# Kernel optimization log

Measured on AMD Instinct MI355X. Metric: run time of the kernel, lower is better.

Reference implementation:

```python
import jax, jax.numpy as jnp
import numpy as np

B, T, DIM, H, BUCKET = 4, 4096, 1024, 16, 64
E = DIM // H          # head dim = 64
U = T // BUCKET       # number of buckets = 64
EPS = 1e-6


def setup_inputs() -> dict:
    key = jax.random.key(0)
    ks = jax.random.split(key, 5)
    scale = 1.0 / np.sqrt(DIM)
    return {
        "x": jax.random.normal(ks[0], (B, T, DIM), dtype=jnp.float32),
        "Wq": jax.random.normal(ks[1], (DIM, DIM), dtype=jnp.float32) * scale,
        "Wk": jax.random.normal(ks[2], (DIM, DIM), dtype=jnp.float32) * scale,
        "Wv": jax.random.normal(ks[3], (DIM, DIM), dtype=jnp.float32) * scale,
        "Wo": jax.random.normal(ks[4], (DIM, DIM), dtype=jnp.float32) * scale,
        "bo": jnp.zeros((DIM,), dtype=jnp.float32),
    }


def _causal_linear_attn(q, k, v):
    # q, k, v: [b, h, t, e]; psi(k) = elu(k) + 1; q softmaxed over feature dim
    q = jax.nn.softmax(q, axis=-1)
    k = jax.nn.elu(k) + 1.0
    bucket = lambda x: x.reshape(*x.shape[:-2], U, BUCKET, E)  # [b,h,u,n,e]
    b_q, b_k, b_v = bucket(q), bucket(k), bucket(v)
    # cumulative key sums per bucket: [b,h,u,d]
    b_k_cumsum = jnp.cumsum(b_k.sum(axis=-2), axis=2)
    # per-bucket context then cumulative over buckets: [b,h,u,d,e]
    context = jnp.einsum("bhund,bhune->bhude", b_k, b_v)
    context = jnp.cumsum(context, axis=2)
    context = context / (b_k_cumsum[..., None] + EPS)
    # shift by one bucket (blindspot): bucket u sees context through bucket u-1
    context = jnp.concatenate(
        [jnp.zeros_like(context[:, :, :1]), context[:, :, :-1]], axis=2
    )
    attn = jnp.einsum("bhund,bhude->bhune", b_q, context)
    return attn.reshape(q.shape)  # [b,h,t,e]


def reference(x, Wq, Wk, Wv, Wo, bo):
    b, t, _ = x.shape
    q = x @ Wq
    k = x @ Wk
    v = x @ Wv
    merge = lambda z: z.reshape(b, t, H, E).transpose(0, 2, 1, 3)  # [b,h,t,e]
    attn = _causal_linear_attn(merge(q), merge(k), merge(v))
    out = attn.transpose(0, 2, 1, 3).reshape(b, t, DIM)
    return out @ Wo + bo
```

## Files before the change

### kernel.cpp

```cpp
#include <hip/hip_runtime.h>


#define T_LEN 4096
#define DIMN  1024
#define NHEAD 16
#define NB    4
#define MROWS (NB * T_LEN)

typedef float f32x4 __attribute__((ext_vector_type(4)));
typedef short s16x8 __attribute__((ext_vector_type(8)));
typedef short s16x4 __attribute__((ext_vector_type(4)));
using u16 = unsigned short;

__device__ __forceinline__ u16 f2bf(float f) {
  unsigned int u = __float_as_uint(f);
  u += 0x7fffu + ((u >> 16) & 1u);
  return (u16)(u >> 16);
}
__device__ __forceinline__ float bf2f(u16 h) {
  return __uint_as_float(((unsigned int)h) << 16);
}
__device__ __forceinline__ int swz16k(int off) {
  return off ^ (((off >> 7) & 3) << 4);
}

__global__ __launch_bounds__(256) void cvt_all_kern(const float* __restrict__ x,
                                                    const float* __restrict__ W0,
                                                    const float* __restrict__ W1,
                                                    const float* __restrict__ W2,
                                                    const float* __restrict__ W3,
                                                    u16* __restrict__ WT,
                                                    u16* __restrict__ xb) {
  __shared__ float tile[64][65];
  const int tid = threadIdx.x;
  if (blockIdx.x < 1024) {
    const int blk = blockIdx.x & 255;
    const int sel = blockIdx.x >> 8;
    const float* W = (sel == 0) ? W0 : (sel == 1) ? W1 : (sel == 2) ? W2 : W3;
    u16* dst = WT + (size_t)sel * DIMN * DIMN;
    const int k0 = (blk >> 4) << 6;
    const int n0 = (blk & 15) << 6;
    const int r = tid >> 6;
    const int c = tid & 63;
#pragma unroll
    for (int i = 0; i < 16; ++i) {
      int row = (i << 2) + r;
      tile[row][c] = W[(size_t)(k0 + row) * DIMN + n0 + c];
    }
    __syncthreads();
#pragma unroll
    for (int i = 0; i < 16; ++i) {
      int row = (i << 2) + r;
      dst[(size_t)(n0 + row) * DIMN + k0 + c] = f2bf(tile[c][row]);
    }
  } else {
    size_t i = ((size_t)(blockIdx.x - 1024) * 256 + tid) * 4;
    f32x4 v = *(const f32x4*)(x + i);
    s16x4 o;
    o.x = (short)f2bf(v.x); o.y = (short)f2bf(v.y);
    o.z = (short)f2bf(v.z); o.w = (short)f2bf(v.w);
    *(s16x4*)(xb + i) = o;
  }
}

template <int MODE>
__global__ __launch_bounds__(512, 4) void gemm_t(
    const u16* __restrict__ A, const u16* __restrict__ Bt,
    u16* __restrict__ dq, u16* __restrict__ dk, u16* __restrict__ dv,
    float* __restrict__ dO, const float* __restrict__ bias) {
  constexpr int K = 1024;
  constexpr int BNT = (MODE == 0) ? 12 : 4;
  constexpr int NT = K / 32;
  __shared__ char lds[73728];

  const int tid = threadIdx.x;
  const int l = tid & 63;
  const int w = tid >> 6;
  const int wm = w >> 2;
  const int wn = w & 3;

  const int xcd = (int)blockIdx.x & 7;
  const int idx = (int)blockIdx.x >> 3;
  const int g = idx / (4 * BNT);
  const int r2 = idx % (4 * BNT);
  const int bn = r2 >> 2;
  const int bm = xcd * 16 + g * 4 + (r2 & 3);
  const size_t arow0 = (size_t)bm * 128;
  const size_t brow0 = (size_t)bn * 256;

  int lrow[2], lcol[2];
#pragma unroll
  for (int i = 0; i < 2; ++i) {
    int lg = swz16k(tid * 16 + i * 8192);
    lrow[i] = lg >> 6;
    lcol[i] = (lg & 63) >> 1;
  }

  const int fr = l & 15;
  const int kswz = (((l >> 4) << 4)) ^ ((((fr >> 1) & 3)) << 4);

  auto STAGE = [&](int buf, int matsel, int tt) {
    const int kbase = (tt & (NT - 1)) * 32;
#pragma unroll
    for (int i = 0; i < 2; ++i) {
      if (matsel == 0 && i == 1) break;
      const u16* src = (matsel == 0)
          ? A  + (arow0 + (size_t)lrow[i]) * K + kbase + lcol[i]
          : Bt + (brow0 + (size_t)lrow[i]) * K + kbase + lcol[i];
      char* dst = lds + (buf * 24576 + matsel * 8192 + i * 8192 + tid * 16);
      __builtin_amdgcn_global_load_lds(
          (__attribute__((address_space(1))) const void*)src,
          (__attribute__((address_space(3))) void*)dst, 16, 0, 0);
    }
  };
  auto LDA = [&](int buf, int rowb) -> s16x8 {
    return *(const s16x8*)(lds + buf * 24576 + rowb * 64 + kswz);
  };
  auto LDB = [&](int buf, int rowb) -> s16x8 {
    return *(const s16x8*)(lds + buf * 24576 + 8192 + rowb * 64 + kswz);
  };

  f32x4 acc[4][4];
#pragma unroll
  for (int i = 0; i < 4; ++i)
#pragma unroll
    for (int j = 0; j < 4; ++j) acc[i][j] = {0.f, 0.f, 0.f, 0.f};

  STAGE(0, 0, 0); STAGE(0, 1, 0);
  STAGE(1, 0, 1); STAGE(1, 1, 1);
  asm volatile("s_waitcnt vmcnt(3)" ::: "memory");
  __builtin_amdgcn_sched_barrier(0);
  __builtin_amdgcn_s_barrier();

  const int amb = wm * 64;
  const int bnb = wn * 64;
  s16x8 af[4], bf[4];

  int bufR = 0, bufW = 2;
#pragma unroll 1
  for (int t = 0; t < NT; ++t) {
    STAGE(bufW, 0, t + 2);
    STAGE(bufW, 1, t + 2);
#pragma unroll
    for (int i = 0; i < 4; ++i) af[i] = LDA(bufR, amb + i * 16 + fr);
#pragma unroll
    for (int i = 0; i < 4; ++i) bf[i] = LDB(bufR, bnb + i * 16 + fr);
    __builtin_amdgcn_s_setprio(1);
#pragma unroll
    for (int mi = 0; mi < 4; ++mi)
#pragma unroll
      for (int ni = 0; ni < 4; ++ni)
        acc[mi][ni] = __builtin_amdgcn_mfma_f32_16x16x32_bf16(
            af[mi], bf[ni], acc[mi][ni], 0, 0, 0);
    __builtin_amdgcn_s_setprio(0);
    asm volatile("s_waitcnt vmcnt(3)" ::: "memory");
    __builtin_amdgcn_sched_barrier(0);
    __builtin_amdgcn_s_barrier();
    bufR = (bufR == 2) ? 0 : bufR + 1;
    bufW = (bufW == 2) ? 0 : bufW + 1;
  }

  const int r0 = (l >> 4) << 2;
  const int c0 = l & 15;
  if constexpr (MODE == 0) {
    const int mat = bn >> 2;
    if (mat == 0) {
      u16* dst = dq;
      const size_t colbase = (size_t)(bn & 3) * 256 + (size_t)wn * 64;
#pragma unroll
      for (int mi = 0; mi < 4; ++mi) {
#pragma unroll
        for (int j = 0; j < 4; ++j) {
          float v0 = acc[mi][0][j], v1 = acc[mi][1][j];
          float v2 = acc[mi][2][j], v3 = acc[mi][3][j];
          float m = fmaxf(fmaxf(v0, v1), fmaxf(v2, v3));
#pragma unroll
          for (int off = 1; off < 16; off <<= 1) m = fmaxf(m, __shfl_xor(m, off));
          float e0 = __expf(v0 - m), e1 = __expf(v1 - m);
          float e2 = __expf(v2 - m), e3 = __expf(v3 - m);
          float s = e0 + e1 + e2 + e3;
#pragma unroll
          for (int off = 1; off < 16; off <<= 1) s += __shfl_xor(s, off);
          float inv = 1.f / s;
          const size_t row = arow0 + wm * 64 + mi * 16 + r0 + j;
          u16* p = dst + row * DIMN + colbase + c0;
          p[0]  = f2bf(e0 * inv); p[16] = f2bf(e1 * inv);
          p[32] = f2bf(e2 * inv); p[48] = f2bf(e3 * inv);
        }
      }
    } else {
      u16* dst = (mat == 1) ? dk : dv;
      const int colb = (bn & 3) * 256 + wn * 64;
#pragma unroll
      for (int mi = 0; mi < 4; ++mi) {
        const size_t row = arow0 + wm * 64 + mi * 16 + r0;
        const int bb = (int)(row >> 12);
        const int t = (int)(row & 4095);
#pragma unroll
        for (int ni = 0; ni < 4; ++ni) {
          const int col = colb + ni * 16 + c0;
          const int h = col >> 6, d = col & 63;
          s16x4 o;
#pragma unroll
          for (int j = 0; j < 4; ++j) {
            float v = acc[mi][ni][j];
            float r = (mat == 1) ? (v > 0.f ? v + 1.f : __expf(v)) : v;
            o[j] = (short)f2bf(r);
          }
          *(s16x4*)&dst[((size_t)((bb * 16 + h) * 64 + d)) * 4096 + t] = o;
        }
      }
    }
  } else {
#pragma unroll
    for (int mi = 0; mi < 4; ++mi)
#pragma unroll
      for (int ni = 0; ni < 4; ++ni) {
        const size_t col = brow0 + (size_t)wn * 64 + ni * 16 + c0;
        const float bv = bias[col];
#pragma unroll
        for (int j = 0; j < 4; ++j) {
          const size_t row = arow0 + wm * 64 + mi * 16 + r0 + j;
          dO[row * DIMN + col] = acc[mi][ni][j] + bv;
        }
      }
  }
}

__global__ __launch_bounds__(256) void ctx_mfma_kern(const u16* __restrict__ kT,
                                                     const u16* __restrict__ vT,
                                                     u16* __restrict__ ctxT,
                                                     float* __restrict__ ksum) {
  const int tid = threadIdx.x;
  const int l = tid & 63;
  const int w = tid >> 6;
  const int bh = (int)blockIdx.x >> 4;
  const int u = (((int)blockIdx.x & 15) << 2) + w;
  const size_t tbase = (size_t)bh * 64 * 4096 + (size_t)u * 64;
  const int fr = l & 15;
  const int kg = (l >> 4) << 3;

  s16x8 a[4][2], b[4][2];
#pragma unroll
  for (int mi = 0; mi < 4; ++mi)
#pragma unroll
    for (int kk = 0; kk < 2; ++kk)
      a[mi][kk] = *(const s16x8*)&vT[tbase + (size_t)(mi * 16 + fr) * 4096 +
                                     kk * 32 + kg];
#pragma unroll
  for (int ni = 0; ni < 4; ++ni)
#pragma unroll
    for (int kk = 0; kk < 2; ++kk)
      b[ni][kk] = *(const s16x8*)&kT[tbase + (size_t)(ni * 16 + fr) * 4096 +
                                     kk * 32 + kg];

  f32x4 acc[4][4];
#pragma unroll
  for (int i = 0; i < 4; ++i)
#pragma unroll
    for (int j = 0; j < 4; ++j) acc[i][j] = {0.f, 0.f, 0.f, 0.f};
#pragma unroll
  for (int mi = 0; mi < 4; ++mi)
#pragma unroll
    for (int ni = 0; ni < 4; ++ni)
#pragma unroll
      for (int kk = 0; kk < 2; ++kk)
        acc[mi][ni] = __builtin_amdgcn_mfma_f32_16x16x32_bf16(
            a[mi][kk], b[ni][kk], acc[mi][ni], 0, 0, 0);

  const size_t kbase = ((size_t)bh * 64 + u) * 64;
#pragma unroll
  for (int ni = 0; ni < 4; ++ni) {
    float s = 0.f;
#pragma unroll
    for (int kk = 0; kk < 2; ++kk)
#pragma unroll
      for (int j = 0; j < 8; ++j) s += bf2f((u16)b[ni][kk][j]);
    s += __shfl_xor(s, 16);
    s += __shfl_xor(s, 32);
    if (l < 16) ksum[kbase + ni * 16 + l] = s;
  }

  const size_t cbase = kbase * 64;
  const int r0 = (l >> 4) << 2;
#pragma unroll
  for (int mi = 0; mi < 4; ++mi)
#pragma unroll
    for (int ni = 0; ni < 4; ++ni)
#pragma unroll
      for (int j = 0; j < 4; ++j)
        ctxT[cbase + (size_t)(mi * 16 + r0 + j) * 64 + ni * 16 + fr] =
            f2bf(acc[mi][ni][j]);
}

__global__ __launch_bounds__(256) void ctx_cumnorm_kern(u16* __restrict__ ctxT,
                                                        const float* __restrict__ ksum) {
  const int tid = blockIdx.x * 256 + threadIdx.x;
  const int bh = tid >> 10;
  const int rem = tid & 1023;
  const int e = rem >> 4;
  const int d0 = (rem & 15) << 2;
  f32x4 c = {0.f, 0.f, 0.f, 0.f};
  f32x4 accK = {0.f, 0.f, 0.f, 0.f};
  for (int u = 0; u < 64; ++u) {
    const size_t cb = (((size_t)(bh * 64 + u)) * 64 + e) * 64 + d0;
    s16x4 raw = *(const s16x4*)&ctxT[cb];
    f32x4 kk = *(const f32x4*)&ksum[((size_t)(bh * 64 + u)) * 64 + d0];
    s16x4 o;
    if (u == 0) {
      o.x = 0; o.y = 0; o.z = 0; o.w = 0;
    } else {
      o.x = (short)f2bf(c.x / (accK.x + 1e-6f));
      o.y = (short)f2bf(c.y / (accK.y + 1e-6f));
      o.z = (short)f2bf(c.z / (accK.z + 1e-6f));
      o.w = (short)f2bf(c.w / (accK.w + 1e-6f));
    }
    *(s16x4*)&ctxT[cb] = o;
    c.x += bf2f((u16)raw.x); c.y += bf2f((u16)raw.y);
    c.z += bf2f((u16)raw.z); c.w += bf2f((u16)raw.w);
    accK += kk;
  }
}

__global__ __launch_bounds__(256) void attn_mfma_kern(const u16* __restrict__ qb,
                                                      const u16* __restrict__ ctxT,
                                                      u16* __restrict__ attn) {
  const int tid = threadIdx.x;
  const int l = tid & 63;
  const int w = tid >> 6;
  const int bh = (int)blockIdx.x >> 4;
  const int u = (((int)blockIdx.x & 15) << 2) + w;
  const int b = bh >> 4, h = bh & 15;
  const size_t rowbase = (size_t)b * T_LEN + (size_t)u * 64;
  const size_t cbase = ((size_t)bh * 64 + u) * 4096;
  const int fr = l & 15;
  const int kg = (l >> 4) << 3;

  s16x8 a[4][2], bfr[4][2];
#pragma unroll
  for (int mi = 0; mi < 4; ++mi)
#pragma unroll
    for (int kk = 0; kk < 2; ++kk)
      a[mi][kk] = *(const s16x8*)&qb[(rowbase + mi * 16 + fr) * DIMN +
                                     (size_t)h * 64 + kk * 32 + kg];
#pragma unroll
  for (int ni = 0; ni < 4; ++ni)
#pragma unroll
    for (int kk = 0; kk < 2; ++kk)
      bfr[ni][kk] = *(const s16x8*)&ctxT[cbase + (size_t)(ni * 16 + fr) * 64 +
                                         kk * 32 + kg];

  f32x4 acc[4][4];
#pragma unroll
  for (int i = 0; i < 4; ++i)
#pragma unroll
    for (int j = 0; j < 4; ++j) acc[i][j] = {0.f, 0.f, 0.f, 0.f};
#pragma unroll
  for (int mi = 0; mi < 4; ++mi)
#pragma unroll
    for (int ni = 0; ni < 4; ++ni)
#pragma unroll
      for (int kk = 0; kk < 2; ++kk)
        acc[mi][ni] = __builtin_amdgcn_mfma_f32_16x16x32_bf16(
            a[mi][kk], bfr[ni][kk], acc[mi][ni], 0, 0, 0);

  const int r0 = (l >> 4) << 2;
#pragma unroll
  for (int mi = 0; mi < 4; ++mi)
#pragma unroll
    for (int ni = 0; ni < 4; ++ni)
#pragma unroll
      for (int j = 0; j < 4; ++j)
        attn[(rowbase + mi * 16 + r0 + j) * DIMN + (size_t)h * 64 +
             ni * 16 + fr] = f2bf(acc[mi][ni][j]);
}

extern "C" void kernel_launch(void* const* d_in, const int* in_sizes, int n_in,
                              void* d_out, int out_size, void* d_ws, size_t ws_size,
                              hipStream_t stream) {
  const float* x  = (const float*)d_in[0];
  const float* Wq = (const float*)d_in[1];
  const float* Wk = (const float*)d_in[2];
  const float* Wv = (const float*)d_in[3];
  const float* Wo = (const float*)d_in[4];
  const float* bo = (const float*)d_in[5];
  float* out = (float*)d_out;

  constexpr size_t SZ_XB = (size_t)MROWS * DIMN * 2;
  constexpr size_t SZ_WT = (size_t)DIMN * DIMN * 2;
  constexpr size_t SZ_CTX = (size_t)NB * NHEAD * 64 * 64 * 64 * 2;
  char* ws = (char*)d_ws;
  u16*   xb   = (u16*)(ws);
  u16*   wqT  = (u16*)(ws + SZ_XB);
  u16*   woT  = (u16*)(ws + SZ_XB + 3 * SZ_WT);
  u16*   qb   = (u16*)(ws + SZ_XB + 4 * SZ_WT);
  u16*   kT   = (u16*)(ws + 2 * SZ_XB + 4 * SZ_WT);
  u16*   vT   = (u16*)(ws + 3 * SZ_XB + 4 * SZ_WT);
  u16*   ctxT = (u16*)(ws + 4 * SZ_XB + 4 * SZ_WT);
  float* ksum = (float*)(ws + 4 * SZ_XB + 4 * SZ_WT + SZ_CTX);
  u16*   attn = xb;

  cvt_all_kern<<<1024 + MROWS * DIMN / 1024, 256, 0, stream>>>(x, Wq, Wk, Wv, Wo,
                                                               wqT, xb);

  gemm_t<0><<<1536, 512, 0, stream>>>(xb, wqT, qb, kT, vT, nullptr, nullptr);

  ctx_mfma_kern<<<NB * NHEAD * 16, 256, 0, stream>>>(kT, vT, ctxT, ksum);
  ctx_cumnorm_kern<<<256, 256, 0, stream>>>(ctxT, ksum);
  attn_mfma_kern<<<NB * NHEAD * 16, 256, 0, stream>>>(qb, ctxT, attn);

  gemm_t<1><<<512, 512, 0, stream>>>(attn, woT, nullptr, nullptr, nullptr, out, bo);
}
```

Baseline: 247.0 us.

## Fuse context, cumulative normalization and attention into one sequential-bucket kernel

Replaces the three middle kernels (per-bucket context MFMA, cumulative sum/normalize, attention MFMA) with one kernel. Each block owns a (batch, head, 16-wide e-slice) and walks the 64 buckets in order, keeping the running context and key sum in registers and staging the normalized previous context through shared memory. This removes the global round-trip of the 32 MB bf16 context tensor and two launches. In exchange it has only 256 blocks, a serial 64-step loop with two barriers per step, and little parallelism per block, so latency may dominate.

```diff
diff --git a/kernel.cpp b/kernel.cpp
--- a/kernel.cpp
+++ b/kernel.cpp
@@ -227,152 +227,93 @@
   }
 }
 
-__global__ __launch_bounds__(256) void ctx_mfma_kern(const u16* __restrict__ kT,
-                                                     const u16* __restrict__ vT,
-                                                     u16* __restrict__ ctxT,
-                                                     float* __restrict__ ksum) {
+__global__ __launch_bounds__(256) void mid_fused_kern(const u16* __restrict__ kT,
+                                                      const u16* __restrict__ vT,
+                                                      const u16* __restrict__ qb,
+                                                      u16* __restrict__ attn) {
+  __shared__ float cprev[16][68];
   const int tid = threadIdx.x;
   const int l = tid & 63;
   const int w = tid >> 6;
-  const int bh = (int)blockIdx.x >> 4;
-  const int u = (((int)blockIdx.x & 15) << 2) + w;
-  const size_t tbase = (size_t)bh * 64 * 4096 + (size_t)u * 64;
   const int fr = l & 15;
-  const int kg = (l >> 4) << 3;
-
-  s16x8 a[4][2], b[4][2];
-#pragma unroll
-  for (int mi = 0; mi < 4; ++mi)
-#pragma unroll
-    for (int kk = 0; kk < 2; ++kk)
-      a[mi][kk] = *(const s16x8*)&vT[tbase + (size_t)(mi * 16 + fr) * 4096 +
-                                     kk * 32 + kg];
-#pragma unroll
-  for (int ni = 0; ni < 4; ++ni)
-#pragma unroll
-    for (int kk = 0; kk < 2; ++kk)
-      b[ni][kk] = *(const s16x8*)&kT[tbase + (size_t)(ni * 16 + fr) * 4096 +
-                                     kk * 32 + kg];
-
-  f32x4 acc[4][4];
-#pragma unroll
-  for (int i = 0; i < 4; ++i)
-#pragma unroll
-    for (int j = 0; j < 4; ++j) acc[i][j] = {0.f, 0.f, 0.f, 0.f};
-#pragma unroll
-  for (int mi = 0; mi < 4; ++mi)
-#pragma unroll
-    for (int ni = 0; ni < 4; ++ni)
-#pragma unroll
-      for (int kk = 0; kk < 2; ++kk)
-        acc[mi][ni] = __builtin_amdgcn_mfma_f32_16x16x32_bf16(
-            a[mi][kk], b[ni][kk], acc[mi][ni], 0, 0, 0);
-
-  const size_t kbase = ((size_t)bh * 64 + u) * 64;
-#pragma unroll
-  for (int ni = 0; ni < 4; ++ni) {
+  const int lg = l >> 4;
+
+  const int bid = (int)blockIdx.x;
+  const int xcd = bid & 7;
+  const int slot = bid >> 3;
+  const int bh = xcd * 8 + (slot >> 2);
+  const int eg = slot & 3;
+  const int b = bh >> 4, h = bh & 15;
+
+  const size_t kvbase = (size_t)bh * 64 * 4096;
+  const size_t qrow0 = (size_t)b * T_LEN;
+
+  auto LV = [&](int u, int kk) -> s16x8 {
+    return *(const s16x8*)&vT[kvbase + (size_t)(eg * 16 + fr) * 4096 +
+                              u * 64 + kk * 32 + lg * 8];
+  };
+  auto LK = [&](int u, int kk) -> s16x8 {
+    return *(const s16x8*)&kT[kvbase + (size_t)(w * 16 + fr) * 4096 +
+                              u * 64 + kk * 32 + lg * 8];
+  };
+  auto LQ = [&](int u, int kk) -> s16x8 {
+    return *(const s16x8*)&qb[(qrow0 + u * 64 + w * 16 + fr) * DIMN +
+                              (size_t)h * 64 + kk * 32 + lg * 8];
+  };
+
+  f32x4 cacc = {0.f, 0.f, 0.f, 0.f};
+  float ksum = 0.f;
+
+  s16x8 vA0 = LV(0, 0), vA1 = LV(0, 1);
+  s16x8 kB0 = LK(0, 0), kB1 = LK(0, 1);
+  s16x8 qA0 = LQ(0, 0), qA1 = LQ(0, 1);
+
+#pragma unroll 1
+  for (int u = 0; u < 64; ++u) {
+    const s16x8 cvA0 = vA0, cvA1 = vA1;
+    const s16x8 ckB0 = kB0, ckB1 = kB1;
+    const s16x8 cqA0 = qA0, cqA1 = qA1;
+    if (u < 63) {
+      vA0 = LV(u + 1, 0); vA1 = LV(u + 1, 1);
+      kB0 = LK(u + 1, 0); kB1 = LK(u + 1, 1);
+      qA0 = LQ(u + 1, 0); qA1 = LQ(u + 1, 1);
+    }
+    const float inv = 1.f / (ksum + 1e-6f);
+#pragma unroll
+    for (int j = 0; j < 4; ++j)
+      cprev[lg * 4 + j][w * 16 + fr] = cacc[j] * inv;
+    __syncthreads();
+    s16x8 cB0, cB1;
+#pragma unroll
+    for (int kk = 0; kk < 2; ++kk) {
+      const float* p = &cprev[fr][kk * 32 + lg * 8];
+      f32x4 lo = *(const f32x4*)p;
+      f32x4 hi = *(const f32x4*)(p + 4);
+      s16x8 t;
+      t[0] = (short)f2bf(lo.x); t[1] = (short)f2bf(lo.y);
+      t[2] = (short)f2bf(lo.z); t[3] = (short)f2bf(lo.w);
+      t[4] = (short)f2bf(hi.x); t[5] = (short)f2bf(hi.y);
+      t[6] = (short)f2bf(hi.z); t[7] = (short)f2bf(hi.w);
+      if (kk == 0) cB0 = t; else cB1 = t;
+    }
+    f32x4 aacc = {0.f, 0.f, 0.f, 0.f};
+    aacc = __builtin_amdgcn_mfma_f32_16x16x32_bf16(cqA0, cB0, aacc, 0, 0, 0);
+    aacc = __builtin_amdgcn_mfma_f32_16x16x32_bf16(cqA1, cB1, aacc, 0, 0, 0);
+    const size_t arow = qrow0 + (size_t)u * 64 + w * 16 + lg * 4;
+#pragma unroll
+    for (int j = 0; j < 4; ++j)
+      attn[(arow + j) * DIMN + (size_t)h * 64 + eg * 16 + fr] = f2bf(aacc[j]);
+    cacc = __builtin_amdgcn_mfma_f32_16x16x32_bf16(cvA0, ckB0, cacc, 0, 0, 0);
+    cacc = __builtin_amdgcn_mfma_f32_16x16x32_bf16(cvA1, ckB1, cacc, 0, 0, 0);
     float s = 0.f;
 #pragma unroll
-    for (int kk = 0; kk < 2; ++kk)
-#pragma unroll
-      for (int j = 0; j < 8; ++j) s += bf2f((u16)b[ni][kk][j]);
+    for (int j = 0; j < 8; ++j)
+      s += bf2f((u16)ckB0[j]) + bf2f((u16)ckB1[j]);
     s += __shfl_xor(s, 16);
     s += __shfl_xor(s, 32);
-    if (l < 16) ksum[kbase + ni * 16 + l] = s;
-  }
-
-  const size_t cbase = kbase * 64;
-  const int r0 = (l >> 4) << 2;
-#pragma unroll
-  for (int mi = 0; mi < 4; ++mi)
-#pragma unroll
-    for (int ni = 0; ni < 4; ++ni)
-#pragma unroll
-      for (int j = 0; j < 4; ++j)
-        ctxT[cbase + (size_t)(mi * 16 + r0 + j) * 64 + ni * 16 + fr] =
-            f2bf(acc[mi][ni][j]);
-}
-
-__global__ __launch_bounds__(256) void ctx_cumnorm_kern(u16* __restrict__ ctxT,
-                                                        const float* __restrict__ ksum) {
-  const int tid = blockIdx.x * 256 + threadIdx.x;
-  const int bh = tid >> 10;
-  const int rem = tid & 1023;
-  const int e = rem >> 4;
-  const int d0 = (rem & 15) << 2;
-  f32x4 c = {0.f, 0.f, 0.f, 0.f};
-  f32x4 accK = {0.f, 0.f, 0.f, 0.f};
-  for (int u = 0; u < 64; ++u) {
-    const size_t cb = (((size_t)(bh * 64 + u)) * 64 + e) * 64 + d0;
-    s16x4 raw = *(const s16x4*)&ctxT[cb];
-    f32x4 kk = *(const f32x4*)&ksum[((size_t)(bh * 64 + u)) * 64 + d0];
-    s16x4 o;
-    if (u == 0) {
-      o.x = 0; o.y = 0; o.z = 0; o.w = 0;
-    } else {
-      o.x = (short)f2bf(c.x / (accK.x + 1e-6f));
-      o.y = (short)f2bf(c.y / (accK.y + 1e-6f));
-      o.z = (short)f2bf(c.z / (accK.z + 1e-6f));
-      o.w = (short)f2bf(c.w / (accK.w + 1e-6f));
-    }
-    *(s16x4*)&ctxT[cb] = o;
-    c.x += bf2f((u16)raw.x); c.y += bf2f((u16)raw.y);
-    c.z += bf2f((u16)raw.z); c.w += bf2f((u16)raw.w);
-    accK += kk;
-  }
-}
-
-__global__ __launch_bounds__(256) void attn_mfma_kern(const u16* __restrict__ qb,
-                                                      const u16* __restrict__ ctxT,
-                                                      u16* __restrict__ attn) {
-  const int tid = threadIdx.x;
-  const int l = tid & 63;
-  const int w = tid >> 6;
-  const int bh = (int)blockIdx.x >> 4;
-  const int u = (((int)blockIdx.x & 15) << 2) + w;
-  const int b = bh >> 4, h = bh & 15;
-  const size_t rowbase = (size_t)b * T_LEN + (size_t)u * 64;
-  const size_t cbase = ((size_t)bh * 64 + u) * 4096;
-  const int fr = l & 15;
-  const int kg = (l >> 4) << 3;
-
-  s16x8 a[4][2], bfr[4][2];
-#pragma unroll
-  for (int mi = 0; mi < 4; ++mi)
-#pragma unroll
-    for (int kk = 0; kk < 2; ++kk)
-      a[mi][kk] = *(const s16x8*)&qb[(rowbase + mi * 16 + fr) * DIMN +
-                                     (size_t)h * 64 + kk * 32 + kg];
-#pragma unroll
-  for (int ni = 0; ni < 4; ++ni)
-#pragma unroll
-    for (int kk = 0; kk < 2; ++kk)
-      bfr[ni][kk] = *(const s16x8*)&ctxT[cbase + (size_t)(ni * 16 + fr) * 64 +
-                                         kk * 32 + kg];
-
-  f32x4 acc[4][4];
-#pragma unroll
-  for (int i = 0; i < 4; ++i)
-#pragma unroll
-    for (int j = 0; j < 4; ++j) acc[i][j] = {0.f, 0.f, 0.f, 0.f};
-#pragma unroll
-  for (int mi = 0; mi < 4; ++mi)
-#pragma unroll
-    for (int ni = 0; ni < 4; ++ni)
-#pragma unroll
-      for (int kk = 0; kk < 2; ++kk)
-        acc[mi][ni] = __builtin_amdgcn_mfma_f32_16x16x32_bf16(
-            a[mi][kk], bfr[ni][kk], acc[mi][ni], 0, 0, 0);
-
-  const int r0 = (l >> 4) << 2;
-#pragma unroll
-  for (int mi = 0; mi < 4; ++mi)
-#pragma unroll
-    for (int ni = 0; ni < 4; ++ni)
-#pragma unroll
-      for (int j = 0; j < 4; ++j)
-        attn[(rowbase + mi * 16 + r0 + j) * DIMN + (size_t)h * 64 +
-             ni * 16 + fr] = f2bf(acc[mi][ni][j]);
+    ksum += s;
+    __syncthreads();
+  }
 }
 
 extern "C" void kernel_launch(void* const* d_in, const int* in_sizes, int n_in,
@@ -388,7 +329,6 @@
 
   constexpr size_t SZ_XB = (size_t)MROWS * DIMN * 2;
   constexpr size_t SZ_WT = (size_t)DIMN * DIMN * 2;
-  constexpr size_t SZ_CTX = (size_t)NB * NHEAD * 64 * 64 * 64 * 2;
   char* ws = (char*)d_ws;
   u16*   xb   = (u16*)(ws);
   u16*   wqT  = (u16*)(ws + SZ_XB);
@@ -396,8 +336,6 @@
   u16*   qb   = (u16*)(ws + SZ_XB + 4 * SZ_WT);
   u16*   kT   = (u16*)(ws + 2 * SZ_XB + 4 * SZ_WT);
   u16*   vT   = (u16*)(ws + 3 * SZ_XB + 4 * SZ_WT);
-  u16*   ctxT = (u16*)(ws + 4 * SZ_XB + 4 * SZ_WT);
-  float* ksum = (float*)(ws + 4 * SZ_XB + 4 * SZ_WT + SZ_CTX);
   u16*   attn = xb;
 
   cvt_all_kern<<<1024 + MROWS * DIMN / 1024, 256, 0, stream>>>(x, Wq, Wk, Wv, Wo,
@@ -405,9 +343,7 @@
 
   gemm_t<0><<<1536, 512, 0, stream>>>(xb, wqT, qb, kT, vT, nullptr, nullptr);
 
-  ctx_mfma_kern<<<NB * NHEAD * 16, 256, 0, stream>>>(kT, vT, ctxT, ksum);
-  ctx_cumnorm_kern<<<256, 256, 0, stream>>>(ctxT, ksum);
-  attn_mfma_kern<<<NB * NHEAD * 16, 256, 0, stream>>>(qb, ctxT, attn);
+  mid_fused_kern<<<256, 256, 0, stream>>>(kT, vT, qb, attn);
 
   gemm_t<1><<<512, 512, 0, stream>>>(attn, woT, nullptr, nullptr, nullptr, out, bo);
 }
```

Result: no change. 247.6 us (+0.2%).
